# Kernel tuning notes

Hardware: AMD Instinct MI355X
Metric: run time of the kernel (lower is better)

Reference implementation:

```python
import jax, jax.numpy as jnp
import numpy as np

# Fixed hierarchical grouping of the 15 regions into 5 groups of 3 (from split_regions)
SPLIT_IDX = np.array([[0, 1, 8], [2, 4, 6], [3, 5, 7], [9, 11, 13], [10, 12, 14]])
BN_EPS = 1e-5


def _bn_relu(x, g, b):
    # BatchNorm over (batch, spatial) dims in training-stats mode, then ReLU
    mu = jnp.mean(x, axis=(0, 2, 3), keepdims=True)
    var = jnp.var(x, axis=(0, 2, 3), keepdims=True)
    xn = (x - mu) * jax.lax.rsqrt(var + BN_EPS)
    return jax.nn.relu(xn * g[None, :, None, None] + b[None, :, None, None])


def _local_agg(x, params):
    # x: [B, Cin, G, K]; pointwise conv (1x1) -> BN -> ReLU per layer, then max over K
    for W, g, b in params:
        x = jnp.einsum('oi,bigk->bogk', W, x)
        x = _bn_relu(x, g, b)
    return jnp.max(x, axis=-1)  # [B, Cout, G]


def setup_inputs() -> dict:
    key = jax.random.key(0)
    ks = jax.random.split(key, 8)
    B, G, K = 32, 15, 2048
    inp = {"local_regions": jax.random.normal(ks[0], (B, G, K, 3), jnp.float32)}
    chans = [(3, 64, 64), (67, 128, 128), (131, 256, 256)]
    ki = 1
    for li, (c0, c1, c2) in enumerate(chans):
        for wi, (co, ci) in enumerate([(c1, c0), (c2, c1)]):
            inp[f"la{li}_w{wi}"] = jax.random.normal(ks[ki], (co, ci), jnp.float32) * (1.0 / np.sqrt(ci))
            inp[f"la{li}_g{wi}"] = jnp.ones((co,), jnp.float32)
            inp[f"la{li}_b{wi}"] = jnp.zeros((co,), jnp.float32)
            ki += 1
    return inp


def reference(local_regions,
              la0_w0, la0_g0, la0_b0, la0_w1, la0_g1, la0_b1,
              la1_w0, la1_g0, la1_b0, la1_w1, la1_g1, la1_b1,
              la2_w0, la2_g0, la2_b0, la2_w1, la2_g1, la2_b1):
    la0 = [(la0_w0, la0_g0, la0_b0), (la0_w1, la0_g1, la0_b1)]
    la1 = [(la1_w0, la1_g0, la1_b0), (la1_w1, la1_g1, la1_b1)]
    la2 = [(la2_w0, la2_g0, la2_b0), (la2_w1, la2_g1, la2_b1)]
    idx = jnp.asarray(SPLIT_IDX)

    x = jnp.transpose(local_regions, (0, 3, 1, 2))  # [B, 3, 15, K]
    centroids_1 = jnp.mean(x, axis=-1)              # [B, 3, 15]
    relative_1 = x - centroids_1[..., None]
    lf1 = _local_agg(relative_1, la0)               # [B, 64, 15]
    local_features = jnp.concatenate([centroids_1, lf1], axis=1)  # [B, 67, 15]

    # level 2: regroup 15 regions into [5, 3]
    lf1_s = jnp.transpose(lf1, (0, 2, 1))[:, idx, :]         # [B, 5, 3, 64]
    lr2 = jnp.transpose(centroids_1, (0, 2, 1))[:, idx, :]   # [B, 5, 3, 3]
    c2 = jnp.mean(lr2, axis=2)                               # [B, 5, 3]
    rel2 = lr2 - c2[:, :, None, :]
    feats2 = jnp.concatenate([rel2, lf1_s], axis=-1)         # [B, 5, 3, 67]
    feats2 = jnp.transpose(feats2, (0, 3, 1, 2))             # [B, 67, 5, 3]
    lf2 = _local_agg(feats2, la1)                            # [B, 128, 5]

    # level 3: global
    c3 = jnp.mean(c2, axis=1)                                # [B, 3]
    rel3 = c2 - c3[:, None, :]                               # [B, 5, 3]
    lf2 = jnp.concatenate([jnp.transpose(rel3, (0, 2, 1)), lf2], axis=1)  # [B, 131, 5]
    lf2 = lf2[:, :, None, :]                                 # [B, 131, 1, 5]
    gf = _local_agg(lf2, la2)                                # [B, 256, 1]
    return gf.squeeze(2), local_features
```

## Files before the change

### kernel.cpp

```cpp
#include <hip/hip_runtime.h>
#include <math.h>

#define GG 15
#define KK 2048
#define NB 480
#define N1F 983040.0f
#define EPS 1e-5f
#define PZN ((int)0xAAAAAAAA)

typedef _Float16 half8 __attribute__((ext_vector_type(8)));
typedef float f32x4 __attribute__((ext_vector_type(4)));

#define CENT  0
#define GSREL 1920
#define GBN1  2160
#define SELO  6256
#define FBN1  36976
#define H2A   37104
#define H2B   98544
#define H3A   159984
#define H3B   200944
#define GS2A  241904
#define GS2B  242416
#define GS3A  242928
#define GS3B  243952
#define CGRP  244976
#define CSUP  247856
#define CFLG  247952

#define SMEMF 7936

__device__ const int SIDX[15] = {0,1,8, 2,4,6, 3,5,7, 9,11,13, 10,12,14};

__device__ __forceinline__ float wave_sum(float v){
    for (int off = 32; off; off >>= 1) v += __shfl_down(v, off, 64);
    return v;
}
__device__ __forceinline__ float aloadf(const float* p){
    return __hip_atomic_load(p, __ATOMIC_RELAXED, __HIP_MEMORY_SCOPE_AGENT);
}
__device__ __forceinline__ int aloadi(const int* p){
    return __hip_atomic_load(p, __ATOMIC_RELAXED, __HIP_MEMORY_SCOPE_AGENT);
}
template<int SLP, class Fold>
__device__ __forceinline__ void gbar2(int* wsi, int idx, int gi, int* sflag,
                                      Fold fold){
    __syncthreads();
    if (threadIdx.x == 0)
        sflag[0] = (atomicAdd(&wsi[CGRP + (idx*30 + gi)*16], 1) == PZN + 15) ? 1 : 0;
    __syncthreads();
    if (sflag[0]) {
        if (threadIdx.x == 0)
            sflag[1] = (atomicAdd(&wsi[CSUP + idx*16], 1) == PZN + 29) ? 1 : 0;
        __syncthreads();
        if (sflag[1]) {
            fold();
            __syncthreads();
            if (threadIdx.x < 30)
                atomicExch(&wsi[CFLG + (idx*30 + threadIdx.x)*16], 1);
        }
    }
    if (threadIdx.x == 0) {
        int g = 0;
        while (aloadi(&wsi[CFLG + (idx*30 + gi)*16]) != 1 && ++g < 8000000)
            __builtin_amdgcn_s_sleep(SLP);
    }
    __syncthreads();
    asm volatile("" ::: "memory");
}
struct NoFold { __device__ void operator()() const {} };

__global__ void __launch_bounds__(256, 2) mega(
        const float* __restrict__ x,
        const float* __restrict__ w00, const float* __restrict__ g00, const float* __restrict__ b00,
        const float* __restrict__ w01, const float* __restrict__ g01, const float* __restrict__ b01,
        const float* __restrict__ w10, const float* __restrict__ g10, const float* __restrict__ b10,
        const float* __restrict__ w11, const float* __restrict__ g11, const float* __restrict__ b11,
        const float* __restrict__ w20, const float* __restrict__ g20, const float* __restrict__ b20,
        const float* __restrict__ w21, const float* __restrict__ g21, const float* __restrict__ b21,
        float* __restrict__ ws, float* __restrict__ out) {
    __shared__ __align__(16) float smemf[SMEMF];
    float* xls  = smemf;
    float* redM = smemf + 6144; float* redN = smemf + 6400;
    float* redS = smemf + 6656; float* redQ = smemf + 6912;
    float* bcast= smemf + 7168;
    int*   sflag= (int*)(smemf + 7916);
    float* s1ls  = smemf;
    float* t1ls  = smemf + 64;
    float* centb = smemf + 128;
    float* c2b   = smemf + 176;
    float* c3b   = smemf + 192;
    float* f2b   = smemf + 256;
    float* wstg  = smemf + 256;
    float* vls   = smemf + 1424;
    float* f3b   = smemf + 3360;
    float* u3b   = smemf + 4020;
    float* c2s   = smemf + 5312;
    float* c2t   = smemf + 5440;
    float* s4ls  = smemf + 5568;
    float* t4ls  = smemf + 5824;
    float* w10st = smemf + 6144;
    float* hst   = smemf + 6912;
    int* wsi = (int*)ws;

    int bid = blockIdx.x, tid = threadIdx.x;
    int b_ = bid / GG, g_ = bid % GG;
    int wv = tid >> 6, lane = tid & 63, l15 = lane & 15, quad = lane >> 4;
    int gi = bid >> 4;
    int sgrp = b_ >> 4;
    int base2 = g_*9,  nr2 = (g_ == 14) ? 2 : 9;
    int base3 = g_*18, nr3 = (g_ == 14) ? 4 : 18;
    int stq = (nr3 < 12) ? nr3 : 12;

    {
        const float4* xp4 = (const float4*)(x + (size_t)bid * KK * 3);
        float4* xls4 = (float4*)xls;
        #pragma unroll
        for (int i = 0; i < 6; i++) xls4[i*256 + tid] = xp4[i*256 + tid];
        __syncthreads();
        float m[9] = {0,0,0,0,0,0,0,0,0};
        float a[24];
        const float* bp = &xls[tid*24];
        #pragma unroll
        for (int i = 0; i < 6; i++)
            *reinterpret_cast<float4*>(&a[i*4]) = *reinterpret_cast<const float4*>(&bp[i*4]);
        #pragma unroll
        for (int p = 0; p < 8; p++) {
            float ax=a[p*3], ay=a[p*3+1], az=a[p*3+2];
            m[0]+=ax; m[1]+=ay; m[2]+=az;
            m[3]=fmaf(ax,ax,m[3]); m[4]=fmaf(ay,ay,m[4]); m[5]=fmaf(az,az,m[5]);
            m[6]=fmaf(ax,ay,m[6]); m[7]=fmaf(ax,az,m[7]); m[8]=fmaf(ay,az,m[8]);
        }
        #pragma unroll
        for (int q = 0; q < 9; q++) {
            float v = wave_sum(m[q]);
            if (lane == 0) redM[q*4 + wv] = v;
        }
        __syncthreads();
        if (tid == 0) {
            float t[9];
            #pragma unroll
            for (int q = 0; q < 9; q++) t[q] = redM[q*4]+redM[q*4+1]+redM[q*4+2]+redM[q*4+3];
            float c0 = t[0]/KK, c1 = t[1]/KK, c2 = t[2]/KK;
            bcast[0]=c0; bcast[1]=c1; bcast[2]=c2;
            out[8192 + b_*(67*GG) + 0*GG + g_] = c0;
            out[8192 + b_*(67*GG) + 1*GG + g_] = c1;
            out[8192 + b_*(67*GG) + 2*GG + g_] = c2;
            atomicExch(&ws[CENT + bid*4 + 0], c0);
            atomicExch(&ws[CENT + bid*4 + 1], c1);
            atomicExch(&ws[CENT + bid*4 + 2], c2);
            redM[40] = t[3] - KK*c0*c0;  redM[41] = t[4] - KK*c1*c1;
            redM[42] = t[5] - KK*c2*c2;  redM[43] = t[6] - KK*c0*c1;
            redM[44] = t[7] - KK*c0*c2;  redM[45] = t[8] - KK*c1*c2;
        }
        __syncthreads();
    }
    if (tid < 6) atomicAdd(&ws[GSREL + gi*8 + tid], redM[40 + tid]);

    half8 afA[4], afB[4];
    #pragma unroll
    for (int t = 0; t < 4; t++)
        #pragma unroll
        for (int j = 0; j < 8; j++) {
            afA[t][j] = (_Float16)w01[(t*16 + l15)*64 + quad*8 + j];
            afB[t][j] = (_Float16)w01[(t*16 + l15)*64 + 32 + quad*8 + j];
        }

    gbar2<4>(wsi, 0, gi, sflag, NoFold{});

    if (tid < 6) {
        float acc = 0.f;
        #pragma unroll
        for (int s = 0; s < 30; s++) acc += aloadf(&ws[GSREL + s*8 + tid]);
        bcast[3+tid] = acc / N1F;
    }
    __syncthreads();
    float c0 = bcast[0], c1 = bcast[1], c2v = bcast[2];
    float S00=bcast[3], S11=bcast[4], S22=bcast[5], S01=bcast[6], S02=bcast[7], S12=bcast[8];

    float wa0[8], wa1[8], wa2[8], ba[8], wb0[8], wb1[8], wb2[8], bb[8];
    #pragma unroll
    for (int j = 0; j < 8; j++) {
        int cA = quad*8 + j;
        float u0=w00[cA*3+0], u1=w00[cA*3+1], u2=w00[cA*3+2];
        float var = u0*u0*S00 + u1*u1*S11 + u2*u2*S22
                  + 2.f*(u0*u1*S01 + u0*u2*S02 + u1*u2*S12);
        float a1 = g00[cA]*rsqrtf(var + EPS);
        wa0[j]=a1*u0; wa1[j]=a1*u1; wa2[j]=a1*u2; ba[j]=b00[cA];
        int cB = cA + 32;
        float v0=w00[cB*3+0], v1=w00[cB*3+1], v2=w00[cB*3+2];
        float varB = v0*v0*S00 + v1*v1*S11 + v2*v2*S22
                   + 2.f*(v0*v1*S01 + v0*v2*S02 + v1*v2*S12);
        float a1B = g00[cB]*rsqrtf(varB + EPS);
        wb0[j]=a1B*v0; wb1[j]=a1B*v1; wb2[j]=a1B*v2; bb[j]=b00[cB];
    }
    float mx[16], mn[16], sm[16], sq[16];
    #pragma unroll
    for (int s = 0; s < 16; s++) { mx[s]=-1e30f; mn[s]=1e30f; sm[s]=0.f; sq[s]=0.f; }

    for (int it = 0; it < 32; it++) {
        int k = it*64 + wv*16 + l15;
        float r0 = xls[k*3+0]-c0, r1 = xls[k*3+1]-c1, r2 = xls[k*3+2]-c2v;
        half8 bf0, bf1;
        #pragma unroll
        for (int j = 0; j < 8; j++) {
            float pA = fmaf(wa0[j],r0, fmaf(wa1[j],r1, fmaf(wa2[j],r2, ba[j])));
            bf0[j] = (_Float16)fmaxf(pA, 0.f);
            float pB = fmaf(wb0[j],r0, fmaf(wb1[j],r1, fmaf(wb2[j],r2, bb[j])));
            bf1[j] = (_Float16)fmaxf(pB, 0.f);
        }
        #pragma unroll
        for (int t = 0; t < 4; t++) {
            f32x4 acc = {0.f,0.f,0.f,0.f};
            acc = __builtin_amdgcn_mfma_f32_16x16x32_f16(afA[t], bf0, acc, 0, 0, 0);
            acc = __builtin_amdgcn_mfma_f32_16x16x32_f16(afB[t], bf1, acc, 0, 0, 0);
            #pragma unroll
            for (int r = 0; r < 4; r++) {
                float h = acc[r];
                int s = t*4 + r;
                mx[s]=fmaxf(mx[s],h); mn[s]=fminf(mn[s],h);
                sm[s]+=h;             sq[s]=fmaf(h,h,sq[s]);
            }
        }
    }
    #pragma unroll
    for (int m = 1; m < 16; m <<= 1) {
        #pragma unroll
        for (int s = 0; s < 16; s++) {
            mx[s] = fmaxf(mx[s], __shfl_xor(mx[s], m, 64));
            mn[s] = fminf(mn[s], __shfl_xor(mn[s], m, 64));
            sm[s] += __shfl_xor(sm[s], m, 64);
            sq[s] += __shfl_xor(sq[s], m, 64);
        }
    }
    __syncthreads();
    if (l15 == 0) {
        #pragma unroll
        for (int t = 0; t < 4; t++)
            #pragma unroll
            for (int r = 0; r < 4; r++) {
                int o = t*16 + quad*4 + r;
                redM[wv*64+o]=mx[t*4+r]; redN[wv*64+o]=mn[t*4+r];
                redS[wv*64+o]=sm[t*4+r]; redQ[wv*64+o]=sq[t*4+r];
            }
    }
    __syncthreads();
    float Mreg = -1e30f, Nreg = 1e30f;
    if (tid < 64) {
        float S=0.f, Q=0.f;
        #pragma unroll
        for (int w = 0; w < 4; w++) {
            Mreg = fmaxf(Mreg, redM[w*64+tid]); Nreg = fminf(Nreg, redN[w*64+tid]);
            S += redS[w*64+tid];               Q += redQ[w*64+tid];
        }
        atomicAdd(&ws[GBN1 + b_*128 + tid], S);
        atomicAdd(&ws[GBN1 + b_*128 + 64 + tid], Q);
        float sel = (g01[tid] >= 0.f) ? Mreg : Nreg;
        atomicExch(&ws[SELO + bid*64 + tid], sel);
    }
    __syncthreads();
    for (int u = tid; u < nr2*67; u += 256) w10st[u] = w10[base2*67 + u];

    gbar2<4>(wsi, 1, gi, sflag, [&]{
        if (tid < 128) {
            float acc = 0.f;
            #pragma unroll
            for (int i = 0; i < 32; i++) acc += aloadf(&ws[GBN1 + i*128 + tid]);
            atomicExch(&ws[FBN1 + tid], acc);
        }
    });

    if (tid < 64) {
        float S = aloadf(&ws[FBN1 + tid]);
        float Q = aloadf(&ws[FBN1 + 64 + tid]);
        float mean = S / N1F;
        float var  = Q / N1F - mean*mean;
        float s1 = g01[tid]*rsqrtf(var + EPS);
        float t1 = b01[tid] - mean*s1;
        float val = fmaxf(fmaf(s1, (s1 >= 0.f) ? Mreg : Nreg, t1), 0.f);
        out[8192 + b_*(67*GG) + (3+tid)*GG + g_] = val;
        s1ls[tid] = s1; t1ls[tid] = t1;
    }

    if (tid < 45) centb[tid] = aloadf(&ws[CENT + (b_*GG + tid/3)*4 + tid%3]);
    __syncthreads();
    if (tid < 15) {
        int s = tid/3, i = tid%3;
        c2b[tid] = (centb[SIDX[s*3+0]*3+i] + centb[SIDX[s*3+1]*3+i]
                  + centb[SIDX[s*3+2]*3+i]) * (1.f/3.f);
    }
    __syncthreads();
    if (tid < 3)
        c3b[tid] = (c2b[tid]+c2b[3+tid]+c2b[6+tid]+c2b[9+tid]+c2b[12+tid]) * 0.2f;
    if (tid < 45) {
        int p = tid/3, i = tid%3;
        f2b[p*69 + i] = centb[SIDX[p]*3+i] - c2b[(p/3)*3 + i];
    }
    for (int u = tid; u < 960; u += 256) {
        int p = u >> 6, ch = u & 63, src = b_*GG + SIDX[p];
        float sel = aloadf(&ws[SELO + src*64 + ch]);
        f2b[p*69 + 3 + ch] = fmaxf(fmaf(s1ls[ch], sel, t1ls[ch]), 0.f);
    }
    __syncthreads();
    if (tid < nr2*15) {
        int rl = tid/15, p = tid%15, r = base2 + rl;
        const float* wr = &w10st[rl*67];
        const float* fp = &f2b[p*69];
        float h = 0.f;
        #pragma unroll 4
        for (int c = 0; c < 67; c++) h = fmaf(wr[c], fp[c], h);
        atomicExch(&ws[H2A + (b_*GG + p)*128 + r], h);
        hst[rl*15 + p] = h;
    }
    __syncthreads();
    if (tid < nr2) {
        int r = base2 + tid;
        float S = 0.f, Q = 0.f;
        #pragma unroll
        for (int p = 0; p < 15; p++) { float v = hst[tid*15+p]; S += v; Q = fmaf(v,v,Q); }
        atomicAdd(&ws[GS2A + sgrp*256 + r], S);
        atomicAdd(&ws[GS2A + sgrp*256 + 128 + r], Q);
    }
    for (int u = tid; u < nr2*128; u += 256)
        wstg[(u>>7)*129 + (u&127)] = w11[base2*128 + u];
    gbar2<1>(wsi, 2, gi, sflag, NoFold{});

    if (tid < 128) {
        float S = aloadf(&ws[GS2A + tid])       + aloadf(&ws[GS2A + 256 + tid]);
        float Q = aloadf(&ws[GS2A + 128 + tid]) + aloadf(&ws[GS2A + 256 + 128 + tid]);
        float mean = S / 480.f, var = Q / 480.f - mean*mean;
        float s2 = g10[tid]*rsqrtf(var + EPS);
        c2s[tid] = s2; c2t[tid] = b10[tid] - mean*s2;
    }
    __syncthreads();
    for (int u = tid; u < 1920; u += 256) {
        int p = u >> 7, ch = u & 127;
        float hv = aloadf(&ws[H2A + (b_*GG + p)*128 + ch]);
        vls[p*129 + ch] = fmaxf(fmaf(c2s[ch], hv, c2t[ch]), 0.f);
    }
    __syncthreads();
    if (tid < nr2*15) {
        int rl = tid/15, p = tid%15, r = base2 + rl;
        const float* wr = &wstg[rl*129];
        const float* vp = &vls[p*129];
        float h = 0.f;
        #pragma unroll 4
        for (int c = 0; c < 128; c++) h = fmaf(wr[c], vp[c], h);
        atomicExch(&ws[H2B + (b_*GG + p)*128 + r], h);
        hst[rl*15 + p] = h;
    }
    __syncthreads();
    if (tid < nr2) {
        int r = base2 + tid;
        float S = 0.f, Q = 0.f;
        #pragma unroll
        for (int p = 0; p < 15; p++) { float v = hst[tid*15+p]; S += v; Q = fmaf(v,v,Q); }
        atomicAdd(&ws[GS2B + sgrp*256 + r], S);
        atomicAdd(&ws[GS2B + sgrp*256 + 128 + r], Q);
    }
    for (int u = tid; u < nr3*131; u += 256) wstg[u] = w20[base3*131 + u];
    gbar2<1>(wsi, 3, gi, sflag, NoFold{});

    if (tid < 128) {
        float S = aloadf(&ws[GS2B + tid])       + aloadf(&ws[GS2B + 256 + tid]);
        float Q = aloadf(&ws[GS2B + 128 + tid]) + aloadf(&ws[GS2B + 256 + 128 + tid]);
        float mean = S / 480.f, var = Q / 480.f - mean*mean;
        float s3 = g11[tid]*rsqrtf(var + EPS);
        c2s[tid] = s3; c2t[tid] = b11[tid] - mean*s3;
    }
    __syncthreads();
    for (int u = tid; u < 640; u += 256) {
        int s = u >> 7, ch = u & 127;
        float sv = c2s[ch], tv = c2t[ch], m = -1e30f;
        #pragma unroll
        for (int j = 0; j < 3; j++) {
            float hv = aloadf(&ws[H2B + (b_*GG + 3*s + j)*128 + ch]);
            m = fmaxf(m, fmaxf(fmaf(sv, hv, tv), 0.f));
        }
        f3b[s*132 + 3 + ch] = m;
    }
    if (tid < 15) {
        int s = tid/3, i = tid%3;
        f3b[s*132 + i] = c2b[tid] - c3b[i];
    }
    __syncthreads();
    if (tid < nr3*5) {
        int rl = tid/5, s = tid%5, r = base3 + rl;
        const float* wr = &wstg[rl*131];
        const float* fp = &f3b[s*132];
        float h = 0.f;
        #pragma unroll 4
        for (int c = 0; c < 131; c++) h = fmaf(wr[c], fp[c], h);
        atomicExch(&ws[H3A + (b_*5 + s)*256 + r], h);
        hst[rl*5 + s] = h;
    }
    __syncthreads();
    if (tid < nr3) {
        int r = base3 + tid;
        float S = 0.f, Q = 0.f;
        #pragma unroll
        for (int s = 0; s < 5; s++) { float v = hst[tid*5+s]; S += v; Q = fmaf(v,v,Q); }
        atomicAdd(&ws[GS3A + sgrp*512 + r], S);
        atomicAdd(&ws[GS3A + sgrp*512 + 256 + r], Q);
    }
    for (int u = tid; u < stq*256; u += 256)
        wstg[(u>>8)*257 + (u&255)] = w21[base3*256 + u];
    gbar2<1>(wsi, 4, gi, sflag, NoFold{});

    {
        float S = aloadf(&ws[GS3A + tid])       + aloadf(&ws[GS3A + 512 + tid]);
        float Q = aloadf(&ws[GS3A + 256 + tid]) + aloadf(&ws[GS3A + 512 + 256 + tid]);
        float mean = S / 160.f, var = Q / 160.f - mean*mean;
        float s4 = g20[tid]*rsqrtf(var + EPS);
        s4ls[tid] = s4; t4ls[tid] = b20[tid] - mean*s4;
    }
    __syncthreads();
    for (int u = tid; u < 1280; u += 256) {
        int s = u >> 8, ch = u & 255;
        float hv = aloadf(&ws[H3A + (b_*5 + s)*256 + ch]);
        u3b[s*257 + ch] = fmaxf(fmaf(s4ls[ch], hv, t4ls[ch]), 0.f);
    }
    __syncthreads();
    if (tid < nr3*5) {
        int rl = tid/5, s = tid%5, r = base3 + rl;
        const float* up = &u3b[s*257];
        float h = 0.f;
        if (rl < 12) {
            const float* wr = &wstg[rl*257];
            #pragma unroll 4
            for (int c = 0; c < 256; c++) h = fmaf(wr[c], up[c], h);
        } else {
            const float* wr = w21 + (size_t)r*256;
            #pragma unroll 4
            for (int c = 0; c < 256; c++) h = fmaf(wr[c], up[c], h);
        }
        atomicExch(&ws[H3B + (b_*5 + s)*256 + r], h);
        hst[rl*5 + s] = h;
    }
    __syncthreads();
    if (tid < nr3) {
        int r = base3 + tid;
        float S = 0.f, Q = 0.f;
        #pragma unroll
        for (int s = 0; s < 5; s++) { float v = hst[tid*5+s]; S += v; Q = fmaf(v,v,Q); }
        atomicAdd(&ws[GS3B + sgrp*512 + r], S);
        atomicAdd(&ws[GS3B + sgrp*512 + 256 + r], Q);
    }
    gbar2<1>(wsi, 5, gi, sflag, NoFold{});

    if (g_ == 0) {
        float S = aloadf(&ws[GS3B + tid])       + aloadf(&ws[GS3B + 512 + tid]);
        float Q = aloadf(&ws[GS3B + 256 + tid]) + aloadf(&ws[GS3B + 512 + 256 + tid]);
        float mean = S / 160.f, var = Q / 160.f - mean*mean;
        float s5 = g21[tid]*rsqrtf(var + EPS);
        float t5 = b21[tid] - mean*s5;
        float m = -1e30f;
        #pragma unroll
        for (int s = 0; s < 5; s++) {
            float hv = aloadf(&ws[H3B + (b_*5 + s)*256 + tid]);
            m = fmaxf(m, fmaxf(fmaf(s5, hv, t5), 0.f));
        }
        out[b_*256 + tid] = m;
    }
}

extern "C" void kernel_launch(void* const* d_in, const int* in_sizes, int n_in,
                              void* d_out, int out_size, void* d_ws, size_t ws_size,
                              hipStream_t stream) {
    (void)in_sizes; (void)n_in; (void)out_size; (void)ws_size;
    const float* x   = (const float*)d_in[0];
    const float* w00 = (const float*)d_in[1];
    const float* g00 = (const float*)d_in[2];
    const float* b00 = (const float*)d_in[3];
    const float* w01 = (const float*)d_in[4];
    const float* g01 = (const float*)d_in[5];
    const float* b01 = (const float*)d_in[6];
    const float* w10 = (const float*)d_in[7];
    const float* g10 = (const float*)d_in[8];
    const float* b10 = (const float*)d_in[9];
    const float* w11 = (const float*)d_in[10];
    const float* g11 = (const float*)d_in[11];
    const float* b11 = (const float*)d_in[12];
    const float* w20 = (const float*)d_in[13];
    const float* g20 = (const float*)d_in[14];
    const float* b20 = (const float*)d_in[15];
    const float* w21 = (const float*)d_in[16];
    const float* g21 = (const float*)d_in[17];
    const float* b21 = (const float*)d_in[18];
    float* out = (float*)d_out;
    float* ws  = (float*)d_ws;

    mega<<<NB, 256, 0, stream>>>(x, w00,g00,b00, w01,g01,b01, w10,g10,b10,
                                 w11,g11,b11, w20,g20,b20, w21,g21,b21, ws, out);
}
```

Measured before the change: 178.0 us.

## Replace hierarchical atomic-counter grid barrier with per-block arrival flags polled by block 0

The two-level grid barrier is replaced. Previously, group counters fed a super counter through atomicAdd and the last arriver ran the fold. Now each block writes its own padded arrival flag, and block 0 polls all 480 flags with its whole thread block, runs the fold, and then releases the 30 group flags. This removes serialized atomic read-modify-write contention and the two-step last-arriver chain. In exchange, block 0 does all the polling, and the new flag region needs a larger workspace that must be reset between launches.

```diff
diff --git a/kernel.cpp b/kernel.cpp
--- a/kernel.cpp
+++ b/kernel.cpp
@@ -24,9 +24,8 @@
 #define GS2B  242416
 #define GS3A  242928
 #define GS3B  243952
-#define CGRP  244976
-#define CSUP  247856
-#define CFLG  247952
+#define CFLG  244976
+#define ARRB  247856
 
 #define SMEMF 7936
 
@@ -43,22 +42,28 @@
     return __hip_atomic_load(p, __ATOMIC_RELAXED, __HIP_MEMORY_SCOPE_AGENT);
 }
 template<int SLP, class Fold>
-__device__ __forceinline__ void gbar2(int* wsi, int idx, int gi, int* sflag,
-                                      Fold fold){
+__device__ __forceinline__ void sbar(int* wsi, int idx, int gi, int bid,
+                                     int* sflag, Fold fold){
     __syncthreads();
     if (threadIdx.x == 0)
-        sflag[0] = (atomicAdd(&wsi[CGRP + (idx*30 + gi)*16], 1) == PZN + 15) ? 1 : 0;
-    __syncthreads();
-    if (sflag[0]) {
-        if (threadIdx.x == 0)
-            sflag[1] = (atomicAdd(&wsi[CSUP + idx*16], 1) == PZN + 29) ? 1 : 0;
+        atomicExch(&wsi[ARRB + (idx*480 + bid)*16], 1);
+    if (bid == 0) {
+        int guard = 0, done = 0;
+        do {
+            int ok = 1;
+            for (int s = threadIdx.x; s < 480; s += 256)
+                ok &= (aloadi(&wsi[ARRB + (idx*480 + s)*16]) == 1) ? 1 : 0;
+            ok = __all(ok) ? 1 : 0;
+            if ((threadIdx.x & 63) == 0) sflag[2 + (threadIdx.x >> 6)] = ok;
+            __syncthreads();
+            done = sflag[2] & sflag[3] & sflag[4] & sflag[5];
+            __syncthreads();
+            if (!done) __builtin_amdgcn_s_sleep(SLP);
+        } while (!done && ++guard < 4000000);
+        fold();
         __syncthreads();
-        if (sflag[1]) {
-            fold();
-            __syncthreads();
-            if (threadIdx.x < 30)
-                atomicExch(&wsi[CFLG + (idx*30 + threadIdx.x)*16], 1);
-        }
+        if (threadIdx.x < 30)
+            atomicExch(&wsi[CFLG + (idx*30 + threadIdx.x)*16], 1);
     }
     if (threadIdx.x == 0) {
         int g = 0;
@@ -166,7 +171,7 @@
             afB[t][j] = (_Float16)w01[(t*16 + l15)*64 + 32 + quad*8 + j];
         }
 
-    gbar2<4>(wsi, 0, gi, sflag, NoFold{});
+    sbar<4>(wsi, 0, gi, bid, sflag, NoFold{});
 
     if (tid < 6) {
         float acc = 0.f;
@@ -261,7 +266,7 @@
     __syncthreads();
     for (int u = tid; u < nr2*67; u += 256) w10st[u] = w10[base2*67 + u];
 
-    gbar2<4>(wsi, 1, gi, sflag, [&]{
+    sbar<4>(wsi, 1, gi, bid, sflag, [&]{
         if (tid < 128) {
             float acc = 0.f;
             #pragma unroll
@@ -323,7 +328,7 @@
     }
     for (int u = tid; u < nr2*128; u += 256)
         wstg[(u>>7)*129 + (u&127)] = w11[base2*128 + u];
-    gbar2<1>(wsi, 2, gi, sflag, NoFold{});
+    sbar<1>(wsi, 2, gi, bid, sflag, NoFold{});
 
     if (tid < 128) {
         float S = aloadf(&ws[GS2A + tid])       + aloadf(&ws[GS2A + 256 + tid]);
@@ -359,7 +364,7 @@
         atomicAdd(&ws[GS2B + sgrp*256 + 128 + r], Q);
     }
     for (int u = tid; u < nr3*131; u += 256) wstg[u] = w20[base3*131 + u];
-    gbar2<1>(wsi, 3, gi, sflag, NoFold{});
+    sbar<1>(wsi, 3, gi, bid, sflag, NoFold{});
 
     if (tid < 128) {
         float S = aloadf(&ws[GS2B + tid])       + aloadf(&ws[GS2B + 256 + tid]);
@@ -405,7 +410,7 @@
     }
     for (int u = tid; u < stq*256; u += 256)
         wstg[(u>>8)*257 + (u&255)] = w21[base3*256 + u];
-    gbar2<1>(wsi, 4, gi, sflag, NoFold{});
+    sbar<1>(wsi, 4, gi, bid, sflag, NoFold{});
 
     {
         float S = aloadf(&ws[GS3A + tid])       + aloadf(&ws[GS3A + 512 + tid]);
@@ -446,7 +451,7 @@
         atomicAdd(&ws[GS3B + sgrp*512 + r], S);
         atomicAdd(&ws[GS3B + sgrp*512 + 256 + r], Q);
     }
-    gbar2<1>(wsi, 5, gi, sflag, NoFold{});
+    sbar<1>(wsi, 5, gi, bid, sflag, NoFold{});
 
     if (g_ == 0) {
         float S = aloadf(&ws[GS3B + tid])       + aloadf(&ws[GS3B + 512 + tid]);
```

Result: no change. 180.2 us (+1.2%).
